# Kernel optimization log

Hardware: AMD Instinct MI355X
Metric: run time of the kernel (lower is better)

The kernel has to match this reference:

```python
import jax, jax.numpy as jnp
import numpy as np

B, L, C, NH = 512, 196, 384, 12
HW = 14  # window side

def _relative_position_index(h, w):
    coords = np.stack(np.meshgrid(np.arange(h), np.arange(w), indexing='ij'))  # [2,h,w]
    cf = coords.reshape(2, -1)                       # [2, L]
    rel = cf[:, :, None] - cf[:, None, :]            # [2, L, L]
    rel = rel.transpose(1, 2, 0).astype(np.int64)    # [L, L, 2]
    rel[..., 0] += h - 1
    rel[..., 1] += w - 1
    rel[..., 0] *= 2 * w - 1
    return rel.sum(-1)                               # [L, L]

def setup_inputs() -> dict:
    key = jax.random.key(0)
    ks = jax.random.split(key, 5)
    hd = C // NH
    x = jax.random.normal(ks[0], (B, L, C), dtype=jnp.float32)
    # weights stored as [in, out] (equivalent to torch Linear weight.T)
    qkv_w = jax.random.normal(ks[1], (C, 3 * C), dtype=jnp.float32) * (C ** -0.5)
    qkv_b = jnp.zeros((3 * C,), dtype=jnp.float32)
    proj_w = jax.random.normal(ks[2], (C, C), dtype=jnp.float32) * (C ** -0.5)
    proj_b = jnp.zeros((C,), dtype=jnp.float32)
    bias_table = jax.random.normal(ks[3], ((2 * HW - 1) ** 2, NH), dtype=jnp.float32) * 0.02
    rel_index = jnp.asarray(_relative_position_index(HW, HW), dtype=jnp.int32)
    return {"x": x, "qkv_w": qkv_w, "qkv_b": qkv_b, "proj_w": proj_w,
            "proj_b": proj_b, "bias_table": bias_table, "rel_index": rel_index}

def reference(x, qkv_w, qkv_b, proj_w, proj_b, bias_table, rel_index):
    b, l, c = x.shape
    nh = bias_table.shape[1]
    hd = c // nh
    scale = hd ** -0.5
    qkv = (x @ qkv_w + qkv_b).reshape(b, l, 3, nh, hd).transpose(2, 0, 3, 1, 4)  # [3,B,nh,L,hd]
    q, k, v = qkv[0] * scale, qkv[1], qkv[2]
    attn = jnp.einsum('bhqd,bhkd->bhqk', q, k)                 # [B,nh,L,L]
    bias = bias_table[rel_index]                               # [L,L,nh]
    attn = attn + bias.transpose(2, 0, 1)[None]                # add [1,nh,L,L]
    attn = jax.nn.softmax(attn, axis=-1)
    out = jnp.einsum('bhqk,bhkd->bhqd', attn, v)               # [B,nh,L,hd]
    out = out.transpose(0, 2, 1, 3).reshape(b, l, c)
    return out @ proj_w + proj_b
```

## Files before the change

kernel.cpp:

```cpp
#include <hip/hip_runtime.h>
#include <hip/hip_bf16.h>
#include <stdint.h>

typedef __hip_bfloat16 bf16;
typedef __attribute__((ext_vector_type(8))) short frag8;
typedef __attribute__((ext_vector_type(4))) float floatx4;

#define B_WIN 512
#define L_TOK 196
#define C_DIM 384
#define NH    12
#define HD    32
#define QP    208
#define KPAD  224
#define VSTR  236
#define QSCALE 0.2550348555f

#if defined(__has_builtin)
#if __has_builtin(__builtin_amdgcn_exp2f)
#define EXP2(x) __builtin_amdgcn_exp2f(x)
#endif
#endif
#ifndef EXP2
#define EXP2(x) exp2f(x)
#endif

__device__ __forceinline__ void async_cp16(const void* g, void* l) {
  __builtin_amdgcn_global_load_lds(
      (const __attribute__((address_space(1))) unsigned int*)g,
      (__attribute__((address_space(3))) unsigned int*)l, 16, 0, 0);
}

__device__ __forceinline__ unsigned short f2bf_bits(float f) {
  bf16 b = __float2bfloat16(f);
  return *(unsigned short*)&b;
}

__global__ void cast_to_bf16(const float* __restrict__ src, bf16* __restrict__ dst) {
  int i = blockIdx.x * 256 + threadIdx.x;
  float4 v = ((const float4*)src)[i];
  ushort4 o;
  o.x = f2bf_bits(v.x); o.y = f2bf_bits(v.y);
  o.z = f2bf_bits(v.z); o.w = f2bf_bits(v.w);
  ((ushort4*)dst)[i] = o;
}

__global__ void transpose_cast(const float* __restrict__ src, bf16* __restrict__ dst,
                               int K, int N) {
  int idx = blockIdx.x * 256 + threadIdx.x;
  if (idx >= K * N) return;
  int k = idx / N, n = idx - k * N;
  dst[n * K + k] = __float2bfloat16(src[idx]);
}

__global__ void bias_fill(const float* __restrict__ table, const int* __restrict__ rel,
                          float* __restrict__ biasf) {
  int idx = blockIdx.x * 256 + threadIdx.x;
  int h = idx / (QP * KPAD);
  int rem = idx - h * (QP * KPAD);
  int q = rem / KPAD, j = rem - q * KPAD;
  int t = j >> 4, qd = (j >> 2) & 3, rr = j & 3;
  int k = (t >> 1) * 32 + qd * 8 + (t & 1) * 4 + rr;
  float v;
  if (q >= L_TOK)      v = 0.f;
  else if (k >= L_TOK) v = -1e30f;
  else                 v = table[rel[q * L_TOK + k] * NH + h] * 1.4426950408889634f;
  biasf[idx] = v;
}

__device__ __forceinline__ void storev(bf16* p, float v)  { *p = __float2bfloat16(v); }
__device__ __forceinline__ void storev(float* p, float v) { *p = v; }

template <typename OT>
__global__ __launch_bounds__(256) void gemm_bt(
    const bf16* __restrict__ A, const bf16* __restrict__ Bt,
    const float* __restrict__ bias, OT* __restrict__ C,
    int M, int N, int K, int lda, int qcols, int nbn, int panel) {
  __shared__ __align__(16) bf16 sA[2][128 * 32];
  __shared__ __align__(16) bf16 sB[2][128 * 32];
  const int tid = threadIdx.x;
  const int wave = tid >> 6, lane = tid & 63;
  const int SUPER = panel * nbn;
  const int bid = blockIdx.x;
  const int sb = bid / SUPER, rsp = bid - sb * SUPER;
  const long bm = (long)(sb * panel + rsp % panel) * 128;
  const long bn = (long)(rsp / panel) * 128;

  const int srow = wave * 32 + (lane >> 2);
  const int scol = (lane & 3) * 8;
  const bf16* gA = A + (bm + srow) * (long)lda + scol;
  const bf16* gB = Bt + (bn + srow) * (long)K + scol;

  floatx4 acc[4][4];
#pragma unroll
  for (int i = 0; i < 4; i++)
#pragma unroll
    for (int j = 0; j < 4; j++) acc[i][j] = (floatx4)(0.f);

  const int wr = (wave & 1) * 64;
  const int wc = (wave >> 1) * 64;

#pragma unroll
  for (int j = 0; j < 2; j++) {
    async_cp16(gA + (size_t)j * 16 * lda, &sA[0][(wave * 32 + j * 16) * 32]);
    async_cp16(gB + (size_t)j * 16 * K, &sB[0][(wave * 32 + j * 16) * 32]);
  }
  __syncthreads();

  int cur = 0;
  for (int k0 = 0; k0 < K; k0 += 32) {
    if (k0 + 32 < K) {
#pragma unroll
      for (int j = 0; j < 2; j++) {
        async_cp16(gA + (size_t)j * 16 * lda + (k0 + 32),
                   &sA[cur ^ 1][(wave * 32 + j * 16) * 32]);
        async_cp16(gB + (size_t)j * 16 * K + (k0 + 32),
                   &sB[cur ^ 1][(wave * 32 + j * 16) * 32]);
      }
    }
    frag8 af[4], bfr[4];
#pragma unroll
    for (int mi = 0; mi < 4; mi++)
      af[mi] = *(const frag8*)&sA[cur][(wr + mi * 16 + (lane & 15)) * 32 + (lane >> 4) * 8];
#pragma unroll
    for (int ni = 0; ni < 4; ni++)
      bfr[ni] = *(const frag8*)&sB[cur][(wc + ni * 16 + (lane & 15)) * 32 + (lane >> 4) * 8];
#pragma unroll
    for (int mi = 0; mi < 4; mi++)
#pragma unroll
      for (int ni = 0; ni < 4; ni++)
        acc[mi][ni] = __builtin_amdgcn_mfma_f32_16x16x32_bf16(af[mi], bfr[ni], acc[mi][ni], 0, 0, 0);
    __syncthreads();
    cur ^= 1;
  }

#pragma unroll
  for (int ni = 0; ni < 4; ni++) {
    const long col = bn + wc + ni * 16 + (lane & 15);
    const float bv = bias[col];
#pragma unroll
    for (int mi = 0; mi < 4; mi++)
#pragma unroll
      for (int r = 0; r < 4; r++) {
        const long row = bm + wr + mi * 16 + (lane >> 4) * 4 + r;
        float val = acc[mi][ni][r] + bv;
        if (col < qcols) val *= QSCALE;
        storev(&C[row * N + col], val);
      }
  }
}

__global__ __launch_bounds__(256) void attn_win(
    bf16* __restrict__ qkv, const float* __restrict__ biasf) {
  __shared__ __align__(16) bf16 kL[KPAD * 32];
  __shared__ __align__(16) bf16 vT[HD * VSTR];
  const int b = blockIdx.x, h = blockIdx.y;
  const int tid = threadIdx.x, wave = tid >> 6, lane = tid & 63;
  bf16* base = qkv + (size_t)b * L_TOK * (3 * C_DIM);

  const int colb = lane & 15;
  const int quad = lane >> 4;
  const int rsub = quad * 4;
  const int kswz = (quad ^ ((colb >> 1) & 3)) * 8;

  const bf16* vbase = base + 2 * C_DIM + h * HD;
  const int i0 = tid;
  const int r0a = i0 >> 2, c8a = (i0 & 3) * 8;
  const bf16* ga = vbase + (size_t)(2 * r0a) * (3 * C_DIM) + c8a;
  uint4 a0 = *(const uint4*)ga;
  uint4 a1 = *(const uint4*)(ga + 3 * C_DIM);
  const int i1 = tid + 256;
  const bool h1 = i1 < 392;
  const int r0b = h1 ? (i1 >> 2) : r0a, c8b = h1 ? (i1 & 3) * 8 : c8a;
  const bf16* gb = vbase + (size_t)(2 * r0b) * (3 * C_DIM) + c8b;
  uint4 b0 = make_uint4(0, 0, 0, 0), b1 = make_uint4(0, 0, 0, 0);
  if (h1) { b0 = *(const uint4*)gb; b1 = *(const uint4*)(gb + 3 * C_DIM); }

  for (int c = wave; c < 14; c += 4) {
    const int j = c * 16 + (lane >> 2);
    const int slot = lane & 3;
    const int t = j >> 4, qd = (j >> 2) & 3, rr = j & 3;
    int k = (t >> 1) * 32 + qd * 8 + (t & 1) * 4 + rr;
    if (k > L_TOK - 1) k = L_TOK - 1;
    const int sj = (j >> 1) & 3;
    const bf16* src = base + (size_t)k * (3 * C_DIM) + C_DIM + h * HD + ((slot ^ sj) * 8);
    async_cp16(src, &kL[c * 512]);
  }

  frag8 aqv[4];
#pragma unroll
  for (int i = 0; i < 4; i++) {
    int rg = wave + 4 * i; if (rg > 12) rg = 12;
    int qrow = rg * 16 + colb; if (qrow > L_TOK - 1) qrow = L_TOK - 1;
    aqv[i] = *(const frag8*)(base + (size_t)qrow * (3 * C_DIM) + h * HD + quad * 8);
  }

  {
    ushort ea0[8], ea1[8];
    *(uint4*)ea0 = a0; *(uint4*)ea1 = a1;
#pragma unroll
    for (int e = 0; e < 8; e++) {
      uint32_t pack = (uint32_t)ea0[e] | ((uint32_t)ea1[e] << 16);
      *(uint32_t*)&vT[(c8a + e) * VSTR + 2 * r0a] = pack;
    }
    if (h1) {
      ushort eb0[8], eb1[8];
      *(uint4*)eb0 = b0; *(uint4*)eb1 = b1;
#pragma unroll
      for (int e = 0; e < 8; e++) {
        uint32_t pack = (uint32_t)eb0[e] | ((uint32_t)eb1[e] << 16);
        *(uint32_t*)&vT[(c8b + e) * VSTR + 2 * r0b] = pack;
      }
    }
  }
  for (int idx = tid; idx < HD * 14; idx += 256) {
    int d = idx / 14, pr = idx - d * 14;
    *(uint32_t*)&vT[d * VSTR + L_TOK + 2 * pr] = 0;
  }
  __syncthreads();

  const float* bB = biasf + (size_t)h * QP * KPAD;

#pragma unroll
  for (int ii = 0; ii < 4; ii++) {
    const int rg = wave + 4 * ii;
    if (rg < 13) {
      const int row0 = rg * 16;
      const float* bR = bB + (size_t)(row0 + colb) * KPAD;

      frag8 ap[7];
      float lsum = 0.f;
#pragma unroll
      for (int kk = 0; kk < 7; kk++) {
        const floatx4 b0v = *(const floatx4*)(bR + (2 * kk) * 16 + rsub);
        const floatx4 b1v = *(const floatx4*)(bR + (2 * kk + 1) * 16 + rsub);
        const frag8 k0 = *(const frag8*)&kL[((2 * kk) * 16 + colb) * 32 + kswz];
        const frag8 k1 = *(const frag8*)&kL[((2 * kk + 1) * 16 + colb) * 32 + kswz];
        floatx4 s0 = __builtin_amdgcn_mfma_f32_16x16x32_bf16(k0, aqv[ii], (floatx4)(0.f), 0, 0, 0);
        floatx4 s1 = __builtin_amdgcn_mfma_f32_16x16x32_bf16(k1, aqv[ii], (floatx4)(0.f), 0, 0, 0);
#pragma unroll
        for (int e = 0; e < 4; e++) {
          float p = EXP2(s0[e] + b0v[e]);
          lsum += p;
          ap[kk][e] = (short)f2bf_bits(p);
        }
#pragma unroll
        for (int e = 0; e < 4; e++) {
          float p = EXP2(s1[e] + b1v[e]);
          lsum += p;
          ap[kk][4 + e] = (short)f2bf_bits(p);
        }
      }
      lsum += __shfl_xor(lsum, 16, 64);
      lsum += __shfl_xor(lsum, 32, 64);
      const float rl = 1.0f / lsum;
      float rln[4];
#pragma unroll
      for (int r = 0; r < 4; r++) rln[r] = __shfl(rl, rsub + r, 64);

      floatx4 o[2] = {(floatx4)(0.f), (floatx4)(0.f)};
#pragma unroll
      for (int kk = 0; kk < 7; kk++)
#pragma unroll
        for (int nt = 0; nt < 2; nt++) {
          const frag8 bv = *(const frag8*)&vT[(nt * 16 + colb) * VSTR + kk * 32 + quad * 8];
          o[nt] = __builtin_amdgcn_mfma_f32_16x16x32_bf16(ap[kk], bv, o[nt], 0, 0, 0);
        }
#pragma unroll
      for (int nt = 0; nt < 2; nt++)
#pragma unroll
        for (int r = 0; r < 4; r++) {
          const int grow = row0 + rsub + r;
          if (grow < L_TOK)
            base[(size_t)grow * (3 * C_DIM) + h * HD + nt * 16 + colb] =
                __float2bfloat16(o[nt][r] * rln[r]);
        }
    }
  }
}

extern "C" void kernel_launch(void* const* d_in, const int* in_sizes, int n_in,
                              void* d_out, int out_size, void* d_ws, size_t ws_size,
                              hipStream_t stream) {
  const float* x      = (const float*)d_in[0];
  const float* qkv_w  = (const float*)d_in[1];
  const float* qkv_b  = (const float*)d_in[2];
  const float* proj_w = (const float*)d_in[3];
  const float* proj_b = (const float*)d_in[4];
  const float* btab   = (const float*)d_in[5];
  const int*   relidx = (const int*)d_in[6];
  float* out = (float*)d_out;

  const size_t M = (size_t)B_WIN * L_TOK;
  char* ws = (char*)d_ws;
  size_t off = 0;
  bf16*  qkv   = (bf16*)(ws + off);  off += M * 1152 * 2;
  bf16*  wT1   = (bf16*)(ws + off);  off += (size_t)1152 * 384 * 2;
  bf16*  wT2   = (bf16*)(ws + off);  off += (size_t)384 * 384 * 2;
  float* biasf = (float*)(ws + off); off += (size_t)NH * QP * KPAD * 4;

  bf16* xb = (ws_size >= off + M * C_DIM * sizeof(bf16))
                 ? (bf16*)(ws + off) : (bf16*)d_out;

  cast_to_bf16<<<(int)(M * C_DIM / 4 / 256), 256, 0, stream>>>(x, xb);
  transpose_cast<<<(384 * 1152 + 255) / 256, 256, 0, stream>>>(qkv_w, wT1, 384, 1152);
  transpose_cast<<<(384 * 384 + 255) / 256, 256, 0, stream>>>(proj_w, wT2, 384, 384);
  bias_fill<<<(NH * QP * KPAD) / 256, 256, 0, stream>>>(btab, relidx, biasf);

  gemm_bt<bf16><<<784 * 9, 256, 0, stream>>>(xb, wT1, qkv_b, qkv,
                                             (int)M, 1152, 384, 384, C_DIM, 9, 28);
  attn_win<<<dim3(B_WIN, NH), 256, 0, stream>>>(qkv, biasf);
  gemm_bt<float><<<784 * 3, 256, 0, stream>>>(qkv, wT2, proj_b, out,
                                              (int)M, 384, 384, 1152, 0, 3, 28);
}
```

Before: 638.2 us.

## Store attention bias in bf16, fuse softmax with PV, use 512-thread blocks

The precomputed relative-position bias is now stored as bf16 in an MFMA-fragment order, so attention reads half as many bias bytes and each lane loads one frag8 per k-tile. The attention kernel moves to 8 waves per block, so each wave handles at most two 16-row groups. The PV MFMA is interleaved into the QK/exp loop, so the whole P matrix is no longer kept in registers, and bias fragments are prefetched three tiles ahead. Rounding the bias to bf16 costs some accuracy, and the larger block with launch bounds (512, 8) could limit registers.

```diff
diff --git a/kernel.cpp b/kernel.cpp
--- a/kernel.cpp
+++ b/kernel.cpp
@@ -36,6 +36,12 @@
   return *(unsigned short*)&b;
 }
 
+__device__ __forceinline__ float bfu2f(short u) {
+  union { uint32_t i; float f; } c;
+  c.i = ((uint32_t)(unsigned short)u) << 16;
+  return c.f;
+}
+
 __global__ void cast_to_bf16(const float* __restrict__ src, bf16* __restrict__ dst) {
   int i = blockIdx.x * 256 + threadIdx.x;
   float4 v = ((const float4*)src)[i];
@@ -54,18 +60,18 @@
 }
 
 __global__ void bias_fill(const float* __restrict__ table, const int* __restrict__ rel,
-                          float* __restrict__ biasf) {
+                          bf16* __restrict__ biasb) {
   int idx = blockIdx.x * 256 + threadIdx.x;
   int h = idx / (QP * KPAD);
   int rem = idx - h * (QP * KPAD);
-  int q = rem / KPAD, j = rem - q * KPAD;
-  int t = j >> 4, qd = (j >> 2) & 3, rr = j & 3;
-  int k = (t >> 1) * 32 + qd * 8 + (t & 1) * 4 + rr;
+  int q = rem / KPAD, r2 = rem - q * KPAD;
+  int kk = r2 >> 5, quad = (r2 >> 3) & 3, i = r2 & 7;
+  int k = kk * 32 + quad * 8 + ((i >= 4) ? 4 : 0) + (i & 3);
   float v;
   if (q >= L_TOK)      v = 0.f;
   else if (k >= L_TOK) v = -1e30f;
   else                 v = table[rel[q * L_TOK + k] * NH + h] * 1.4426950408889634f;
-  biasf[idx] = v;
+  biasb[idx] = __float2bfloat16(v);
 }
 
 __device__ __forceinline__ void storev(bf16* p, float v)  { *p = __float2bfloat16(v); }
@@ -150,8 +156,8 @@
   }
 }
 
-__global__ __launch_bounds__(256) void attn_win(
-    bf16* __restrict__ qkv, const float* __restrict__ biasf) {
+__global__ __launch_bounds__(512, 8) void attn_win(
+    bf16* __restrict__ qkv, const bf16* __restrict__ biasb) {
   __shared__ __align__(16) bf16 kL[KPAD * 32];
   __shared__ __align__(16) bf16 vT[HD * VSTR];
   const int b = blockIdx.x, h = blockIdx.y;
@@ -164,19 +170,16 @@
   const int kswz = (quad ^ ((colb >> 1) & 3)) * 8;
 
   const bf16* vbase = base + 2 * C_DIM + h * HD;
-  const int i0 = tid;
-  const int r0a = i0 >> 2, c8a = (i0 & 3) * 8;
-  const bf16* ga = vbase + (size_t)(2 * r0a) * (3 * C_DIM) + c8a;
-  uint4 a0 = *(const uint4*)ga;
-  uint4 a1 = *(const uint4*)(ga + 3 * C_DIM);
-  const int i1 = tid + 256;
-  const bool h1 = i1 < 392;
-  const int r0b = h1 ? (i1 >> 2) : r0a, c8b = h1 ? (i1 & 3) * 8 : c8a;
-  const bf16* gb = vbase + (size_t)(2 * r0b) * (3 * C_DIM) + c8b;
-  uint4 b0 = make_uint4(0, 0, 0, 0), b1 = make_uint4(0, 0, 0, 0);
-  if (h1) { b0 = *(const uint4*)gb; b1 = *(const uint4*)(gb + 3 * C_DIM); }
-
-  for (int c = wave; c < 14; c += 4) {
+  const int r0a = tid >> 2, c8a = (tid & 3) * 8;
+  const bool hv = tid < 392;
+  uint4 a0 = make_uint4(0, 0, 0, 0), a1 = make_uint4(0, 0, 0, 0);
+  if (hv) {
+    const bf16* ga = vbase + (size_t)(2 * r0a) * (3 * C_DIM) + c8a;
+    a0 = *(const uint4*)ga;
+    a1 = *(const uint4*)(ga + 3 * C_DIM);
+  }
+
+  for (int c = wave; c < 14; c += 8) {
     const int j = c * 16 + (lane >> 2);
     const int slot = lane & 3;
     const int t = j >> 4, qd = (j >> 2) & 3, rr = j & 3;
@@ -187,15 +190,22 @@
     async_cp16(src, &kL[c * 512]);
   }
 
-  frag8 aqv[4];
-#pragma unroll
-  for (int i = 0; i < 4; i++) {
-    int rg = wave + 4 * i; if (rg > 12) rg = 12;
-    int qrow = rg * 16 + colb; if (qrow > L_TOK - 1) qrow = L_TOK - 1;
-    aqv[i] = *(const frag8*)(base + (size_t)qrow * (3 * C_DIM) + h * HD + quad * 8);
-  }
-
+  frag8 aq0, aq1;
   {
+    int q0 = wave * 16 + colb;
+    aq0 = *(const frag8*)(base + (size_t)q0 * (3 * C_DIM) + h * HD + quad * 8);
+    int rg1 = wave + 8; if (rg1 > 12) rg1 = 12;
+    int q1 = rg1 * 16 + colb; if (q1 > L_TOK - 1) q1 = L_TOK - 1;
+    aq1 = *(const frag8*)(base + (size_t)q1 * (3 * C_DIM) + h * HD + quad * 8);
+  }
+
+  const bf16* biasB = biasb + (size_t)h * QP * KPAD;
+  const bf16* bRow0 = biasB + (size_t)(wave * 16 + colb) * KPAD;
+  frag8 p00 = *(const frag8*)&bRow0[0 * 32 + quad * 8];
+  frag8 p01 = *(const frag8*)&bRow0[1 * 32 + quad * 8];
+  frag8 p02 = *(const frag8*)&bRow0[2 * 32 + quad * 8];
+
+  if (hv) {
     ushort ea0[8], ea1[8];
     *(uint4*)ea0 = a0; *(uint4*)ea1 = a1;
 #pragma unroll
@@ -203,79 +213,67 @@
       uint32_t pack = (uint32_t)ea0[e] | ((uint32_t)ea1[e] << 16);
       *(uint32_t*)&vT[(c8a + e) * VSTR + 2 * r0a] = pack;
     }
-    if (h1) {
-      ushort eb0[8], eb1[8];
-      *(uint4*)eb0 = b0; *(uint4*)eb1 = b1;
-#pragma unroll
-      for (int e = 0; e < 8; e++) {
-        uint32_t pack = (uint32_t)eb0[e] | ((uint32_t)eb1[e] << 16);
-        *(uint32_t*)&vT[(c8b + e) * VSTR + 2 * r0b] = pack;
-      }
+  }
+  if (tid < HD * 14) {
+    int d = tid / 14, pr = tid - d * 14;
+    *(uint32_t*)&vT[d * VSTR + L_TOK + 2 * pr] = 0;
+  }
+  __syncthreads();
+
+  auto rg_body = [&](int rg, frag8 aq, const bf16* bRow,
+                     frag8 b0, frag8 b1, frag8 b2) {
+    const int row0 = rg * 16;
+    frag8 bb[7];
+    bb[0] = b0; bb[1] = b1; bb[2] = b2;
+    floatx4 o0 = (floatx4)(0.f), o1 = (floatx4)(0.f);
+    float lsum = 0.f;
+#pragma unroll
+    for (int kk = 0; kk < 7; kk++) {
+      const frag8 k0 = *(const frag8*)&kL[((2 * kk) * 16 + colb) * 32 + kswz];
+      const frag8 k1 = *(const frag8*)&kL[((2 * kk + 1) * 16 + colb) * 32 + kswz];
+      floatx4 s0 = __builtin_amdgcn_mfma_f32_16x16x32_bf16(k0, aq, (floatx4)(0.f), 0, 0, 0);
+      floatx4 s1 = __builtin_amdgcn_mfma_f32_16x16x32_bf16(k1, aq, (floatx4)(0.f), 0, 0, 0);
+      if (kk + 3 < 7) bb[kk + 3] = *(const frag8*)&bRow[(kk + 3) * 32 + quad * 8];
+      frag8 ap;
+#pragma unroll
+      for (int e = 0; e < 4; e++) {
+        float p = EXP2(s0[e] + bfu2f(bb[kk][e]));
+        lsum += p;
+        ap[e] = (short)f2bf_bits(p);
+      }
+#pragma unroll
+      for (int e = 0; e < 4; e++) {
+        float p = EXP2(s1[e] + bfu2f(bb[kk][4 + e]));
+        lsum += p;
+        ap[4 + e] = (short)f2bf_bits(p);
+      }
+      const frag8 bv0 = *(const frag8*)&vT[colb * VSTR + kk * 32 + quad * 8];
+      const frag8 bv1 = *(const frag8*)&vT[(16 + colb) * VSTR + kk * 32 + quad * 8];
+      o0 = __builtin_amdgcn_mfma_f32_16x16x32_bf16(ap, bv0, o0, 0, 0, 0);
+      o1 = __builtin_amdgcn_mfma_f32_16x16x32_bf16(ap, bv1, o1, 0, 0, 0);
     }
-  }
-  for (int idx = tid; idx < HD * 14; idx += 256) {
-    int d = idx / 14, pr = idx - d * 14;
-    *(uint32_t*)&vT[d * VSTR + L_TOK + 2 * pr] = 0;
-  }
-  __syncthreads();
-
-  const float* bB = biasf + (size_t)h * QP * KPAD;
-
-#pragma unroll
-  for (int ii = 0; ii < 4; ii++) {
-    const int rg = wave + 4 * ii;
-    if (rg < 13) {
-      const int row0 = rg * 16;
-      const float* bR = bB + (size_t)(row0 + colb) * KPAD;
-
-      frag8 ap[7];
-      float lsum = 0.f;
-#pragma unroll
-      for (int kk = 0; kk < 7; kk++) {
-        const floatx4 b0v = *(const floatx4*)(bR + (2 * kk) * 16 + rsub);
-        const floatx4 b1v = *(const floatx4*)(bR + (2 * kk + 1) * 16 + rsub);
-        const frag8 k0 = *(const frag8*)&kL[((2 * kk) * 16 + colb) * 32 + kswz];
-        const frag8 k1 = *(const frag8*)&kL[((2 * kk + 1) * 16 + colb) * 32 + kswz];
-        floatx4 s0 = __builtin_amdgcn_mfma_f32_16x16x32_bf16(k0, aqv[ii], (floatx4)(0.f), 0, 0, 0);
-        floatx4 s1 = __builtin_amdgcn_mfma_f32_16x16x32_bf16(k1, aqv[ii], (floatx4)(0.f), 0, 0, 0);
-#pragma unroll
-        for (int e = 0; e < 4; e++) {
-          float p = EXP2(s0[e] + b0v[e]);
-          lsum += p;
-          ap[kk][e] = (short)f2bf_bits(p);
-        }
-#pragma unroll
-        for (int e = 0; e < 4; e++) {
-          float p = EXP2(s1[e] + b1v[e]);
-          lsum += p;
-          ap[kk][4 + e] = (short)f2bf_bits(p);
-        }
-      }
-      lsum += __shfl_xor(lsum, 16, 64);
-      lsum += __shfl_xor(lsum, 32, 64);
-      const float rl = 1.0f / lsum;
-      float rln[4];
-#pragma unroll
-      for (int r = 0; r < 4; r++) rln[r] = __shfl(rl, rsub + r, 64);
-
-      floatx4 o[2] = {(floatx4)(0.f), (floatx4)(0.f)};
-#pragma unroll
-      for (int kk = 0; kk < 7; kk++)
-#pragma unroll
-        for (int nt = 0; nt < 2; nt++) {
-          const frag8 bv = *(const frag8*)&vT[(nt * 16 + colb) * VSTR + kk * 32 + quad * 8];
-          o[nt] = __builtin_amdgcn_mfma_f32_16x16x32_bf16(ap[kk], bv, o[nt], 0, 0, 0);
-        }
-#pragma unroll
-      for (int nt = 0; nt < 2; nt++)
-#pragma unroll
-        for (int r = 0; r < 4; r++) {
-          const int grow = row0 + rsub + r;
-          if (grow < L_TOK)
-            base[(size_t)grow * (3 * C_DIM) + h * HD + nt * 16 + colb] =
-                __float2bfloat16(o[nt][r] * rln[r]);
-        }
+    lsum += __shfl_xor(lsum, 16, 64);
+    lsum += __shfl_xor(lsum, 32, 64);
+    const float rl = 1.0f / lsum;
+#pragma unroll
+    for (int r = 0; r < 4; r++) {
+      const float rn = __shfl(rl, rsub + r, 64);
+      const int grow = row0 + rsub + r;
+      if (grow < L_TOK) {
+        base[(size_t)grow * (3 * C_DIM) + h * HD + colb] = __float2bfloat16(o0[r] * rn);
+        base[(size_t)grow * (3 * C_DIM) + h * HD + 16 + colb] = __float2bfloat16(o1[r] * rn);
+      }
     }
+  };
+
+  rg_body(wave, aq0, bRow0, p00, p01, p02);
+  if (wave < 5) {
+    const int rg1 = wave + 8;
+    const bf16* bRow1 = biasB + (size_t)(rg1 * 16 + colb) * KPAD;
+    frag8 q0 = *(const frag8*)&bRow1[0 * 32 + quad * 8];
+    frag8 q1 = *(const frag8*)&bRow1[1 * 32 + quad * 8];
+    frag8 q2 = *(const frag8*)&bRow1[2 * 32 + quad * 8];
+    rg_body(rg1, aq1, bRow1, q0, q1, q2);
   }
 }
 
@@ -297,7 +295,7 @@
   bf16*  qkv   = (bf16*)(ws + off);  off += M * 1152 * 2;
   bf16*  wT1   = (bf16*)(ws + off);  off += (size_t)1152 * 384 * 2;
   bf16*  wT2   = (bf16*)(ws + off);  off += (size_t)384 * 384 * 2;
-  float* biasf = (float*)(ws + off); off += (size_t)NH * QP * KPAD * 4;
+  bf16*  biasb = (bf16*)(ws + off);  off += (size_t)NH * QP * KPAD * 2;
 
   bf16* xb = (ws_size >= off + M * C_DIM * sizeof(bf16))
                  ? (bf16*)(ws + off) : (bf16*)d_out;
@@ -305,11 +303,11 @@
   cast_to_bf16<<<(int)(M * C_DIM / 4 / 256), 256, 0, stream>>>(x, xb);
   transpose_cast<<<(384 * 1152 + 255) / 256, 256, 0, stream>>>(qkv_w, wT1, 384, 1152);
   transpose_cast<<<(384 * 384 + 255) / 256, 256, 0, stream>>>(proj_w, wT2, 384, 384);
-  bias_fill<<<(NH * QP * KPAD) / 256, 256, 0, stream>>>(btab, relidx, biasf);
+  bias_fill<<<(NH * QP * KPAD) / 256, 256, 0, stream>>>(btab, relidx, biasb);
 
   gemm_bt<bf16><<<784 * 9, 256, 0, stream>>>(xb, wT1, qkv_b, qkv,
                                              (int)M, 1152, 384, 384, C_DIM, 9, 28);
-  attn_win<<<dim3(B_WIN, NH), 256, 0, stream>>>(qkv, biasf);
+  attn_win<<<dim3(B_WIN, NH), 512, 0, stream>>>(qkv, biasb);
   gemm_bt<float><<<784 * 3, 256, 0, stream>>>(qkv, wT2, proj_b, out,
                                               (int)M, 384, 384, 1152, 0, 3, 28);
 }
```

After: 1.049 ms. 64.4% more time.
